# Kernel tuning notes

Hardware: AMD Instinct MI355X
Metric: run time of the kernel (lower is better)

## Reference

```python
import jax, jax.numpy as jnp
import numpy as np

N, E = 25000, 400000
D, H, L = 64, 4, 3
DH = D  # per-head out dim (concat=False averages heads)
NODE_IN, EDGE_IN = 16, 4


def setup_inputs() -> dict:
    key = jax.random.key(0)
    ks = jax.random.split(key, 24)
    s = 0.05
    inp = {
        "node_feat_in": jax.random.normal(ks[0], (N, NODE_IN), jnp.float32),
        "edge_index_in": jax.random.randint(ks[1], (2, E), 0, N, jnp.int32),
        "edge_attr_in": jax.random.normal(ks[2], (E, EDGE_IN), jnp.float32),
        # initial embeddings
        "W_node": jax.random.normal(ks[3], (NODE_IN, D), jnp.float32) * s,
        "b_node": jnp.zeros((D,), jnp.float32),
        "W_edge": jax.random.normal(ks[4], (EDGE_IN, D), jnp.float32) * s,
        "b_edge": jnp.zeros((D,), jnp.float32),
        # GATv2Conv params, stacked over layers
        "Wl": jax.random.normal(ks[5], (L, D, H * DH), jnp.float32) * s,
        "bl": jnp.zeros((L, H * DH), jnp.float32),
        "Wr": jax.random.normal(ks[6], (L, D, H * DH), jnp.float32) * s,
        "br": jnp.zeros((L, H * DH), jnp.float32),
        "We": jax.random.normal(ks[7], (L, D, H * DH), jnp.float32) * s,
        "att": jax.random.normal(ks[8], (L, H, DH), jnp.float32) * s,
        "conv_b": jnp.zeros((L, D), jnp.float32),
        # LayerNorm
        "ln_g": jnp.ones((L, D), jnp.float32),
        "ln_b": jnp.zeros((L, D), jnp.float32),
        # edge update MLP: Linear(3D->D), ReLU, Linear(D->D)
        "euW1": jax.random.normal(ks[9], (L, 3 * D, D), jnp.float32) * s,
        "eub1": jnp.zeros((L, D), jnp.float32),
        "euW2": jax.random.normal(ks[10], (L, D, D), jnp.float32) * s,
        "eub2": jnp.zeros((L, D), jnp.float32),
    }
    return inp


def _layernorm(x, g, b, eps=1e-5):
    mu = x.mean(-1, keepdims=True)
    var = ((x - mu) ** 2).mean(-1, keepdims=True)
    return (x - mu) * jax.lax.rsqrt(var + eps) * g + b


def _gatv2_conv(x, e, row, col, Wl, bl, Wr, br, We, att, cb):
    # PyG GATv2Conv(concat=False, edge_dim=D), eval mode (no dropout),
    # add_self_loops=True with fill_value='mean' on edge_attr.
    n = x.shape[0]
    xl = (x @ Wl + bl).reshape(n, H, DH)  # source transform
    xr = (x @ Wr + br).reshape(n, H, DH)  # target transform
    # self-loop edge attr = per-target mean of incoming edge attrs
    cnt = jax.ops.segment_sum(jnp.ones((e.shape[0],), x.dtype), col, num_segments=n)
    e_loop = jax.ops.segment_sum(e, col, num_segments=n) / jnp.maximum(cnt, 1.0)[:, None]
    ee = (jnp.concatenate([e, e_loop], 0) @ We).reshape(-1, H, DH)
    loop = jnp.arange(n, dtype=row.dtype)
    rowf = jnp.concatenate([row, loop])
    colf = jnp.concatenate([col, loop])
    msg = xl[rowf] + xr[colf] + ee                      # [E+N, H, DH]
    score = jnp.sum(jax.nn.leaky_relu(msg, 0.2) * att, -1)  # [E+N, H]
    # segment softmax over incoming edges of each target node
    m = jax.ops.segment_max(score, colf, num_segments=n)
    a = jnp.exp(score - m[colf])
    a = a / jax.ops.segment_sum(a, colf, num_segments=n)[colf]
    out = jax.ops.segment_sum(a[..., None] * xl[rowf], colf, num_segments=n)  # [N,H,DH]
    return out.mean(1) + cb  # concat=False -> head mean, plus bias


def reference(node_feat_in, edge_index_in, edge_attr_in, W_node, b_node, W_edge,
              b_edge, Wl, bl, Wr, br, We, att, conv_b, ln_g, ln_b, euW1, eub1,
              euW2, eub2):
    row, col = edge_index_in[0], edge_index_in[1]
    x = jax.nn.relu(node_feat_in @ W_node + b_node)
    e = jax.nn.relu(edge_attr_in @ W_edge + b_edge)
    for i in range(L):
        upd = _gatv2_conv(x, e, row, col, Wl[i], bl[i], Wr[i], br[i], We[i],
                          att[i], conv_b[i])
        x = jax.nn.relu(_layernorm(x + upd, ln_g[i], ln_b[i]))
        eu_in = jnp.concatenate([x[row], x[col], e], -1)  # [E, 3D]
        e_upd = jax.nn.relu(eu_in @ euW1[i] + eub1[i]) @ euW2[i] + eub2[i]
        e = jax.nn.relu(e + e_upd)
    return x, e
```

## Files before the change

### kernel.cpp

```cpp
#include <hip/hip_runtime.h>
#include <hip/hip_bf16.h>
#include <cstdint>
#include <cstddef>

constexpr int kN  = 25000;
constexpr int kE  = 400000;
constexpr int kEN = kE + kN;
constexpr int kD  = 64;
constexpr int kH  = 4;
constexpr int kHD = 256;

typedef __attribute__((ext_vector_type(8))) short short8;
typedef __attribute__((ext_vector_type(4))) float f32x4;

__device__ __forceinline__ float lrelu02(float x){ return x > 0.f ? x : 0.2f*x; }
__device__ __forceinline__ unsigned short f2bf(float f){
  __hip_bfloat16 h = __float2bfloat16(f);
  return *reinterpret_cast<unsigned short*>(&h);
}
__device__ __forceinline__ float bf2f(unsigned short u){
  return __uint_as_float(((unsigned)u) << 16);
}
__device__ __forceinline__ float bf_lo(unsigned u){ return __uint_as_float(u << 16); }
__device__ __forceinline__ float bf_hi(unsigned u){ return __uint_as_float(u & 0xffff0000u); }
__device__ __forceinline__ unsigned pack_bf2(float a, float b){
  return ((unsigned)f2bf(a)) | (((unsigned)f2bf(b)) << 16);
}

__global__ void k_deg(const int* __restrict__ col, int* __restrict__ deg){
  int i = blockIdx.x*256 + threadIdx.x;
  if (i < kE) atomicAdd(&deg[col[i]], 1);
}

__global__ void k_scan(const int* __restrict__ deg, int* __restrict__ col_start){
  __shared__ int lds[1024];
  __shared__ int carry_s;
  int t = threadIdx.x;
  if (t == 0) carry_s = 0;
  __syncthreads();
  for (int base = 0; base < kN; base += 1024){
    int v = (base + t < kN) ? deg[base + t] : 0;
    lds[t] = v; __syncthreads();
    for (int off = 1; off < 1024; off <<= 1){
      int add = (t >= off) ? lds[t - off] : 0;
      __syncthreads();
      lds[t] += add;
      __syncthreads();
    }
    int incl = lds[t];
    int carry = carry_s;
    if (base + t < kN) col_start[base + t] = carry + incl - v;
    __syncthreads();
    if (t == 0) carry_s = carry + lds[1023];
    __syncthreads();
  }
  if (t == 0) col_start[kN] = carry_s;
}

__global__ void k_fill(const int* __restrict__ col, const int* __restrict__ col_start,
                       int* __restrict__ fill, int* __restrict__ edge_ids){
  int i = blockIdx.x*256 + threadIdx.x;
  if (i < kE){
    int c = col[i];
    int p = atomicAdd(&fill[c], 1);
    edge_ids[col_start[c] + p] = i;
  }
}

__global__ void k_permrc(const int* __restrict__ edge_ids, const int* __restrict__ row,
                         const int* __restrict__ col, int* __restrict__ rowp,
                         int2* __restrict__ rc2){
  int p = blockIdx.x*256 + threadIdx.x;
  if (p < kE){
    int eid = edge_ids[p];
    int r = row[eid], c = col[eid];
    rowp[p] = r;
    rc2[p] = make_int2(r, c);
  }
}

__global__ void k_prep(const float* __restrict__ We, unsigned short* __restrict__ WeT){
  int idx = blockIdx.x*256 + threadIdx.x;
  if (idx >= 3*256*64) return;
  int l = idx >> 14, j = (idx >> 6) & 255, k = idx & 63;
  WeT[idx] = f2bf(We[(size_t)l*16384 + k*256 + j]);
}

__global__ void k_prep2(const float* __restrict__ euW1, const float* __restrict__ euW2,
                        unsigned short* __restrict__ W1cT, unsigned short* __restrict__ W2T){
  int idx = blockIdx.x*256 + threadIdx.x;
  if (idx >= 3*64*64) return;
  int l = idx >> 12, rem = idx & 4095, d = rem >> 6, k = rem & 63;
  W1cT[idx] = f2bf(euW1[(size_t)l*192*64 + (size_t)(128+k)*64 + d]);
  W2T[idx]  = f2bf(euW2[(size_t)l*64*64  + (size_t)k*64 + d]);
}

__global__ void k_x0(const float* __restrict__ nf, const float* __restrict__ W,
                     const float* __restrict__ b, float* __restrict__ x){
  int i = blockIdx.x*256 + threadIdx.x;
  if (i >= kN*kD) return;
  int n = i >> 6, d = i & 63;
  float acc = b[d];
#pragma unroll
  for (int k = 0; k < 16; k++) acc += nf[n*16 + k] * W[k*64 + d];
  x[i] = fmaxf(acc, 0.f);
}

__global__ void k_e0p(const int* __restrict__ edge_ids,
                      const float* __restrict__ ea, const float* __restrict__ W,
                      const float* __restrict__ b,
                      unsigned short* __restrict__ ebf_perm){
  long long i = (long long)blockIdx.x*256 + threadIdx.x;
  if (i >= (long long)kE*kD) return;
  int p = (int)(i >> 6), d = (int)(i & 63);
  int eid = edge_ids[p];
  float acc = b[d];
#pragma unroll
  for (int k = 0; k < 4; k++) acc += ea[eid*4 + k] * W[k*64 + d];
  ebf_perm[i] = f2bf(fmaxf(acc, 0.f));
}

#define XLR_NPB 8
__global__ __launch_bounds__(256) void k_xlr(const float* __restrict__ x,
    const float* __restrict__ Wl, const float* __restrict__ bl,
    const float* __restrict__ Wr, const float* __restrict__ br,
    unsigned short* __restrict__ xl_bf, unsigned short* __restrict__ xr_bf){
  __shared__ float xs[XLR_NPB*64];
  int j = threadIdx.x;
  int n0 = blockIdx.x * XLR_NPB;
  for (int i = j; i < XLR_NPB*64; i += 256){
    int n = n0 + (i >> 6);
    xs[i] = (n < kN) ? x[(size_t)n*64 + (i & 63)] : 0.f;
  }
  __syncthreads();
  float accl[XLR_NPB], accr[XLR_NPB];
  float blv = bl[j], brv = br[j];
#pragma unroll
  for (int t = 0; t < XLR_NPB; t++){ accl[t] = blv; accr[t] = brv; }
  for (int k = 0; k < 64; k++){
    float wl = Wl[k*kHD + j], wr = Wr[k*kHD + j];
#pragma unroll
    for (int t = 0; t < XLR_NPB; t++){
      float xv = xs[t*64 + k];
      accl[t] += xv * wl; accr[t] += xv * wr;
    }
  }
#pragma unroll
  for (int t = 0; t < XLR_NPB; t++){
    int n = n0 + t;
    if (n < kN){
      xl_bf[(size_t)n*kHD + j] = f2bf(accl[t]);
      xr_bf[(size_t)n*kHD + j] = f2bf(accr[t]);
    }
  }
}

__global__ __launch_bounds__(256) void k_eloop(const unsigned short* __restrict__ ebf_perm,
    const int* __restrict__ col_start, unsigned short* __restrict__ eloop_bf){
  int wave = threadIdx.x >> 6, lane = threadIdx.x & 63;
  int n = blockIdx.x*4 + wave;
  if (n >= kN) return;
  int s0 = col_start[n], s1 = col_start[n+1];
  float acc = 0.f;
  for (int p = s0; p < s1; p++)
    acc += bf2f(ebf_perm[(size_t)p*64 + lane]);
  int dg = s1 - s0;
  eloop_bf[(size_t)n*64 + lane] = f2bf(acc / (float)(dg > 0 ? dg : 1));
}

struct STile {
  short8 b0, b1;
  uint2 xlu[4], xru[4];
};

__device__ __forceinline__ void s_load(int tile, STile& f, int e16, int kb, int h,
    const unsigned short* __restrict__ ebf_perm,
    const unsigned short* __restrict__ eloop_bf,
    const unsigned short* __restrict__ xl_bf,
    const unsigned short* __restrict__ xr_bf,
    const int2* __restrict__ rc2)
{
  int p = tile*16 + e16;
  int pc = (p < kEN) ? p : 0;
  bool isE = pc < kE;
  int2 rc;
  if (isE) rc = rc2[pc];
  else { rc.x = pc - kE; rc.y = pc - kE; }
  const unsigned short* erow = isE ? (ebf_perm + (size_t)pc*64)
                                   : (eloop_bf + (size_t)(pc - kE)*64);
  f.b0 = *(const short8*)(erow + kb*8);
  f.b1 = *(const short8*)(erow + 32 + kb*8);
  const unsigned short* xl_ = xl_bf + (size_t)rc.x*kHD + h*64;
  const unsigned short* xr_ = xr_bf + (size_t)rc.y*kHD + h*64;
#pragma unroll
  for (int mt = 0; mt < 4; mt++){
    f.xlu[mt] = *(const uint2*)(xl_ + mt*16 + kb*4);
    f.xru[mt] = *(const uint2*)(xr_ + mt*16 + kb*4);
  }
}

__device__ __forceinline__ void s_comp(int tile, const STile& f,
    const short8 A[4][2], const uint2 attp[4], int lane, int h,
    float* __restrict__ score)
{
  float sc = 0.f;
#pragma unroll
  for (int mt = 0; mt < 4; mt++){
    f32x4 acc = {0.f,0.f,0.f,0.f};
    acc = __builtin_amdgcn_mfma_f32_16x16x32_bf16(A[mt][0], f.b0, acc, 0, 0, 0);
    acc = __builtin_amdgcn_mfma_f32_16x16x32_bf16(A[mt][1], f.b1, acc, 0, 0, 0);
    sc += lrelu02(acc[0] + bf_lo(f.xlu[mt].x) + bf_lo(f.xru[mt].x)) * bf_lo(attp[mt].x);
    sc += lrelu02(acc[1] + bf_hi(f.xlu[mt].x) + bf_hi(f.xru[mt].x)) * bf_hi(attp[mt].x);
    sc += lrelu02(acc[2] + bf_lo(f.xlu[mt].y) + bf_lo(f.xru[mt].y)) * bf_lo(attp[mt].y);
    sc += lrelu02(acc[3] + bf_hi(f.xlu[mt].y) + bf_hi(f.xru[mt].y)) * bf_hi(attp[mt].y);
  }
  sc += __shfl_xor(sc, 16);
  sc += __shfl_xor(sc, 32);
  int wp = tile*16 + lane;
  if (lane < 16 && wp < kEN) score[(size_t)wp*kH + h] = sc;
}

__global__ __launch_bounds__(256) void k_score_mfma(
    const unsigned short* __restrict__ ebf_perm,
    const unsigned short* __restrict__ eloop_bf,
    const unsigned short* __restrict__ xl_bf,
    const unsigned short* __restrict__ xr_bf,
    const int2* __restrict__ rc2,
    const unsigned short* __restrict__ WeT,
    const float* __restrict__ att,
    float* __restrict__ score)
{
  int lane = threadIdx.x & 63;
  int h    = threadIdx.x >> 6;
  int e16  = lane & 15;
  int kb   = lane >> 4;

  short8 A[4][2];
  uint2 attp[4];
#pragma unroll
  for (int mt = 0; mt < 4; mt++){
    const unsigned short* arow = WeT + (size_t)(h*64 + mt*16 + e16)*64 + kb*8;
    A[mt][0] = *(const short8*)(arow);
    A[mt][1] = *(const short8*)(arow + 32);
    f32x4 av = *(const f32x4*)(att + h*64 + mt*16 + kb*4);
    attp[mt].x = pack_bf2(av[0], av[1]);
    attp[mt].y = pack_bf2(av[2], av[3]);
  }

  constexpr int NT = (kEN + 15)/16;
  const int G = gridDim.x;
  STile fA, fB;
  int t0 = blockIdx.x;
  if (t0 < NT) s_load(t0, fA, e16, kb, h, ebf_perm, eloop_bf, xl_bf, xr_bf, rc2);
  for (int tile = t0; tile < NT; tile += 2*G){
    int t1 = tile + G;
    if (t1 < NT) s_load(t1, fB, e16, kb, h, ebf_perm, eloop_bf, xl_bf, xr_bf, rc2);
    s_comp(tile, fA, A, attp, lane, h, score);
    if (t1 < NT){
      int t2 = tile + 2*G;
      if (t2 < NT) s_load(t2, fA, e16, kb, h, ebf_perm, eloop_bf, xl_bf, xr_bf, rc2);
      s_comp(t1, fB, A, attp, lane, h, score);
    }
  }
}

__global__ __launch_bounds__(256) void k_agg_ln(
    const unsigned short* __restrict__ xl_bf, const float* __restrict__ score,
    const int* __restrict__ rowp, const int* __restrict__ col_start,
    const float* __restrict__ conv_b, const float* __restrict__ ln_g,
    const float* __restrict__ ln_b, float* __restrict__ x){
  int wv = threadIdx.x >> 6, l = threadIdx.x & 63;
  int n = blockIdx.x*4 + wv;
  if (n >= kN) return;
  int h = l >> 4;
  int s0 = col_start[n], s1 = col_start[n+1];

  float sc_self = score[(size_t)(kE + n)*kH + h];
  float m = sc_self;
  for (int p = s0; p < s1; p++)
    m = fmaxf(m, score[(size_t)p*kH + h]);

  float w0 = __expf(sc_self - m);
  float s = w0;
  float a0, a1, a2, a3;
  {
    uint2 u = *(const uint2*)(xl_bf + (size_t)n*kHD + l*4);
    a0 = w0*bf_lo(u.x); a1 = w0*bf_hi(u.x);
    a2 = w0*bf_lo(u.y); a3 = w0*bf_hi(u.y);
  }
  int p = s0;
  for (; p + 4 <= s1; p += 4){
    float e0 = __expf(score[(size_t)(p+0)*kH + h] - m);
    float e1 = __expf(score[(size_t)(p+1)*kH + h] - m);
    float e2 = __expf(score[(size_t)(p+2)*kH + h] - m);
    float e3 = __expf(score[(size_t)(p+3)*kH + h] - m);
    int r0 = rowp[p], r1 = rowp[p+1], r2 = rowp[p+2], r3 = rowp[p+3];
    uint2 u0 = *(const uint2*)(xl_bf + (size_t)r0*kHD + l*4);
    uint2 u1 = *(const uint2*)(xl_bf + (size_t)r1*kHD + l*4);
    uint2 u2 = *(const uint2*)(xl_bf + (size_t)r2*kHD + l*4);
    uint2 u3 = *(const uint2*)(xl_bf + (size_t)r3*kHD + l*4);
    s += e0 + e1 + e2 + e3;
    a0 += e0*bf_lo(u0.x) + e1*bf_lo(u1.x) + e2*bf_lo(u2.x) + e3*bf_lo(u3.x);
    a1 += e0*bf_hi(u0.x) + e1*bf_hi(u1.x) + e2*bf_hi(u2.x) + e3*bf_hi(u3.x);
    a2 += e0*bf_lo(u0.y) + e1*bf_lo(u1.y) + e2*bf_lo(u2.y) + e3*bf_lo(u3.y);
    a3 += e0*bf_hi(u0.y) + e1*bf_hi(u1.y) + e2*bf_hi(u2.y) + e3*bf_hi(u3.y);
  }
  for (; p < s1; p++){
    float ew = __expf(score[(size_t)p*kH + h] - m);
    int r = rowp[p];
    uint2 u = *(const uint2*)(xl_bf + (size_t)r*kHD + l*4);
    s += ew;
    a0 += ew*bf_lo(u.x); a1 += ew*bf_hi(u.x);
    a2 += ew*bf_lo(u.y); a3 += ew*bf_hi(u.y);
  }
  float inv = 1.f / s;
  a0 *= inv; a1 *= inv; a2 *= inv; a3 *= inv;
  a0 += __shfl_xor(a0, 16); a0 += __shfl_xor(a0, 32);
  a1 += __shfl_xor(a1, 16); a1 += __shfl_xor(a1, 32);
  a2 += __shfl_xor(a2, 16); a2 += __shfl_xor(a2, 32);
  a3 += __shfl_xor(a3, 16); a3 += __shfl_xor(a3, 32);
  int d0 = (l & 15)*4;
  f32x4 cb = *(const f32x4*)(conv_b + d0);
  f32x4 xv = *(const f32x4*)(x + (size_t)n*64 + d0);
  float y0 = xv[0] + a0*0.25f + cb[0];
  float y1 = xv[1] + a1*0.25f + cb[1];
  float y2 = xv[2] + a2*0.25f + cb[2];
  float y3 = xv[3] + a3*0.25f + cb[3];
  float part = y0 + y1 + y2 + y3;
  part += __shfl_xor(part, 1); part += __shfl_xor(part, 2);
  part += __shfl_xor(part, 4); part += __shfl_xor(part, 8);
  float mu = part * (1.f/64.f);
  float f0 = y0 - mu, f1 = y1 - mu, f2 = y2 - mu, f3 = y3 - mu;
  float vp = f0*f0 + f1*f1 + f2*f2 + f3*f3;
  vp += __shfl_xor(vp, 1); vp += __shfl_xor(vp, 2);
  vp += __shfl_xor(vp, 4); vp += __shfl_xor(vp, 8);
  float rstd = rsqrtf(vp * (1.f/64.f) + 1e-5f);
  f32x4 gv = *(const f32x4*)(ln_g + d0);
  f32x4 bv = *(const f32x4*)(ln_b + d0);
  if (l < 16){
    f32x4 o;
    o[0] = fmaxf(f0*rstd*gv[0] + bv[0], 0.f);
    o[1] = fmaxf(f1*rstd*gv[1] + bv[1], 0.f);
    o[2] = fmaxf(f2*rstd*gv[2] + bv[2], 0.f);
    o[3] = fmaxf(f3*rstd*gv[3] + bv[3], 0.f);
    *(f32x4*)(x + (size_t)n*64 + d0) = o;
  }
}

#define PQ_NPB 16
__global__ __launch_bounds__(256) void k_pq(const float* __restrict__ x,
    const float* __restrict__ W1, const float* __restrict__ b1,
    unsigned short* __restrict__ P_bf, unsigned short* __restrict__ Q_bf){
  __shared__ float xs[PQ_NPB*64];
  int tid = threadIdx.x;
  int j = tid & 63;
  int s = tid >> 6;
  int n0 = blockIdx.x * PQ_NPB;
  for (int i = tid; i < PQ_NPB*64; i += 256){
    int n = n0 + (i >> 6);
    xs[i] = (n < kN) ? x[(size_t)n*64 + (i & 63)] : 0.f;
  }
  __syncthreads();
  float accP[4], accQ[4];
  float b1v = b1[j];
#pragma unroll
  for (int t = 0; t < 4; t++){ accP[t] = b1v; accQ[t] = 0.f; }
  for (int k = 0; k < 64; k++){
    float wa = W1[k*64 + j];
    float wb = W1[(64 + k)*64 + j];
#pragma unroll
    for (int t = 0; t < 4; t++){
      float xv = xs[(s*4 + t)*64 + k];
      accP[t] += xv * wa; accQ[t] += xv * wb;
    }
  }
#pragma unroll
  for (int t = 0; t < 4; t++){
    int n = n0 + s*4 + t;
    if (n < kN){
      P_bf[(size_t)n*64 + j] = f2bf(accP[t]);
      Q_bf[(size_t)n*64 + j] = f2bf(accQ[t]);
    }
  }
}

__global__ __launch_bounds__(256) void k_mlp_mfma(
    unsigned short* __restrict__ ebf_perm,
    float* __restrict__ eout_scatter,
    const int* __restrict__ edge_ids,
    const unsigned short* __restrict__ P_bf, const unsigned short* __restrict__ Q_bf,
    const unsigned short* __restrict__ W1cT,
    const unsigned short* __restrict__ W2T,
    const float* __restrict__ b2,
    const int2* __restrict__ rc2)
{
  __shared__ unsigned short Hl[4][1024];
  int lane = threadIdx.x & 63, wv = threadIdx.x >> 6;
  int e16 = lane & 15, g = lane >> 4;
  int swz = (e16 & 7) << 4;
  char* Hw = (char*)Hl[wv];
  bool last = (eout_scatter != nullptr);

  short8 a1[4][2], a2[4][2];
#pragma unroll
  for (int mt = 0; mt < 4; mt++){
#pragma unroll
    for (int c = 0; c < 2; c++){
      a1[mt][c] = *(const short8*)(W1cT + (size_t)(mt*16 + e16)*64 + c*32 + g*8);
      a2[mt][c] = *(const short8*)(W2T  + (size_t)(mt*16 + e16)*64 + c*32 + g*8);
    }
  }
  f32x4 b2v[4];
#pragma unroll
  for (int mt = 0; mt < 4; mt++) b2v[mt] = *(const f32x4*)(b2 + mt*16 + g*4);

  int wid = (blockIdx.x*256 + threadIdx.x) >> 6;
  int nw  = (gridDim.x*256) >> 6;
  for (int tile = wid; tile < kE/16; tile += nw){
    int p = tile*16 + e16;
    int2 rc = rc2[p];
    const unsigned short* erow = ebf_perm + (size_t)p*64;
    short8 eb0 = *(const short8*)(erow + g*8);
    short8 eb1 = *(const short8*)(erow + 32 + g*8);
    const unsigned short* Pr = P_bf + (size_t)rc.x*64;
    const unsigned short* Qc = Q_bf + (size_t)rc.y*64;

#pragma unroll
    for (int mt = 0; mt < 4; mt++){
      f32x4 acc = {0.f,0.f,0.f,0.f};
      acc = __builtin_amdgcn_mfma_f32_16x16x32_bf16(a1[mt][0], eb0, acc, 0, 0, 0);
      acc = __builtin_amdgcn_mfma_f32_16x16x32_bf16(a1[mt][1], eb1, acc, 0, 0, 0);
      uint2 pu = *(const uint2*)(Pr + mt*16 + g*4);
      uint2 qu = *(const uint2*)(Qc + mt*16 + g*4);
      float h0 = fmaxf(acc[0] + bf_lo(pu.x) + bf_lo(qu.x), 0.f);
      float h1 = fmaxf(acc[1] + bf_hi(pu.x) + bf_hi(qu.x), 0.f);
      float h2 = fmaxf(acc[2] + bf_lo(pu.y) + bf_lo(qu.y), 0.f);
      float h3 = fmaxf(acc[3] + bf_hi(pu.y) + bf_hi(qu.y), 0.f);
      uint2 pk; pk.x = pack_bf2(h0, h1); pk.y = pack_bf2(h2, h3);
      *(uint2*)(Hw + (((e16 << 7) + (mt << 5) + (g << 3)) ^ swz)) = pk;
    }
    short8 hb0 = *(const short8*)(Hw + (((e16 << 7)      + (g << 4)) ^ swz));
    short8 hb1 = *(const short8*)(Hw + (((e16 << 7) + 64 + (g << 4)) ^ swz));

    int oe = last ? edge_ids[p] : 0;
#pragma unroll
    for (int mt = 0; mt < 4; mt++){
      f32x4 o = {0.f,0.f,0.f,0.f};
      o = __builtin_amdgcn_mfma_f32_16x16x32_bf16(a2[mt][0], hb0, o, 0, 0, 0);
      o = __builtin_amdgcn_mfma_f32_16x16x32_bf16(a2[mt][1], hb1, o, 0, 0, 0);
      size_t off = (size_t)p*64 + mt*16 + g*4;
      uint2 u = *(const uint2*)(ebf_perm + off);
      f32x4 eo;
      eo[0] = bf_lo(u.x); eo[1] = bf_hi(u.x); eo[2] = bf_lo(u.y); eo[3] = bf_hi(u.y);
      f32x4 ne;
      ne[0] = fmaxf(eo[0] + o[0] + b2v[mt][0], 0.f);
      ne[1] = fmaxf(eo[1] + o[1] + b2v[mt][1], 0.f);
      ne[2] = fmaxf(eo[2] + o[2] + b2v[mt][2], 0.f);
      ne[3] = fmaxf(eo[3] + o[3] + b2v[mt][3], 0.f);
      if (!last){
        uint2 po; po.x = pack_bf2(ne[0], ne[1]); po.y = pack_bf2(ne[2], ne[3]);
        *(uint2*)(ebf_perm + off) = po;
      } else {
        *(f32x4*)(eout_scatter + (size_t)oe*64 + mt*16 + g*4) = ne;
      }
    }
  }
}

extern "C" void kernel_launch(void* const* d_in, const int* in_sizes, int n_in,
                              void* d_out, int out_size, void* d_ws, size_t ws_size,
                              hipStream_t stream) {
  const float* node_feat = (const float*)d_in[0];
  const int*   edge_idx  = (const int*)d_in[1];
  const float* edge_attr = (const float*)d_in[2];
  const float* W_node = (const float*)d_in[3];
  const float* b_node = (const float*)d_in[4];
  const float* W_edge = (const float*)d_in[5];
  const float* b_edge = (const float*)d_in[6];
  const float* Wl   = (const float*)d_in[7];
  const float* bl   = (const float*)d_in[8];
  const float* Wr   = (const float*)d_in[9];
  const float* br   = (const float*)d_in[10];
  const float* We   = (const float*)d_in[11];
  const float* att  = (const float*)d_in[12];
  const float* cvb  = (const float*)d_in[13];
  const float* lng  = (const float*)d_in[14];
  const float* lnb  = (const float*)d_in[15];
  const float* euW1 = (const float*)d_in[16];
  const float* eub1 = (const float*)d_in[17];
  const float* euW2 = (const float*)d_in[18];
  const float* eub2 = (const float*)d_in[19];

  const int* row = edge_idx;
  const int* col = edge_idx + kE;

  float* x = (float*)d_out;
  float* e_out = (float*)d_out + (size_t)kN*kD;

  char* p = (char*)d_ws;
  auto carve = [&](size_t bytes)->void*{
    void* r = (void*)p;
    p += (bytes + 255) & ~(size_t)255;
    return r;
  };
  unsigned short* xl_bf    = (unsigned short*)carve((size_t)kN*kHD*2);
  unsigned short* xr_bf    = (unsigned short*)carve((size_t)kN*kHD*2);
  unsigned short* P_bf     = (unsigned short*)carve((size_t)kN*kD*2);
  unsigned short* Q_bf     = (unsigned short*)carve((size_t)kN*kD*2);
  unsigned short* ebf_perm = (unsigned short*)carve((size_t)kE*kD*2);
  unsigned short* eloop_bf = (unsigned short*)carve((size_t)kN*kD*2);
  unsigned short* WeT      = (unsigned short*)carve((size_t)3*kHD*kD*2);
  unsigned short* W1cT     = (unsigned short*)carve((size_t)3*kD*kD*2);
  unsigned short* W2T      = (unsigned short*)carve((size_t)3*kD*kD*2);
  float* score  = (float*)carve((size_t)kEN*kH*4);
  int* deg      = (int*)carve((size_t)kN*4);
  int* col_start= (int*)carve((size_t)(kN+1)*4);
  int* fill     = (int*)carve((size_t)kN*4);
  int* edge_ids = (int*)carve((size_t)kE*4);
  int* rowp     = (int*)carve((size_t)kE*4);
  int2* rc2     = (int2*)carve((size_t)kE*8);

  hipMemsetAsync(deg, 0, (size_t)kN*4, stream);
  hipMemsetAsync(fill, 0, (size_t)kN*4, stream);
  k_deg<<<(kE+255)/256, 256, 0, stream>>>(col, deg);
  k_scan<<<1, 1024, 0, stream>>>(deg, col_start);
  k_fill<<<(kE+255)/256, 256, 0, stream>>>(col, col_start, fill, edge_ids);
  k_permrc<<<(kE+255)/256, 256, 0, stream>>>(edge_ids, row, col, rowp, rc2);

  k_prep<<<192, 256, 0, stream>>>(We, WeT);
  k_prep2<<<48, 256, 0, stream>>>(euW1, euW2, W1cT, W2T);
  k_x0<<<(kN*kD+255)/256, 256, 0, stream>>>(node_feat, W_node, b_node, x);
  k_e0p<<<(int)(((size_t)kE*kD+255)/256), 256, 0, stream>>>(edge_ids, edge_attr, W_edge,
                                                            b_edge, ebf_perm);

  for (int i = 0; i < 3; i++){
    const float* Wl_i  = Wl  + (size_t)i*kD*kHD;
    const float* bl_i  = bl  + (size_t)i*kHD;
    const float* Wr_i  = Wr  + (size_t)i*kD*kHD;
    const float* br_i  = br  + (size_t)i*kHD;
    const float* att_i = att + (size_t)i*kHD;
    const float* cvb_i = cvb + (size_t)i*kD;
    const float* lng_i = lng + (size_t)i*kD;
    const float* lnb_i = lnb + (size_t)i*kD;
    const float* W1_i  = euW1 + (size_t)i*192*64;
    const float* b1_i  = eub1 + (size_t)i*kD;
    const float* b2_i  = eub2 + (size_t)i*kD;
    const unsigned short* WeT_i  = WeT  + (size_t)i*kHD*kD;
    const unsigned short* W1cT_i = W1cT + (size_t)i*kD*kD;
    const unsigned short* W2T_i  = W2T  + (size_t)i*kD*kD;

    k_xlr<<<(kN + XLR_NPB - 1)/XLR_NPB, 256, 0, stream>>>(x, Wl_i, bl_i, Wr_i, br_i,
                                                          xl_bf, xr_bf);
    k_eloop<<<(kN + 3)/4, 256, 0, stream>>>(ebf_perm, col_start, eloop_bf);
    k_score_mfma<<<2048, 256, 0, stream>>>(ebf_perm, eloop_bf, xl_bf, xr_bf,
                                           rc2, WeT_i, att_i, score);
    k_agg_ln<<<(kN + 3)/4, 256, 0, stream>>>(xl_bf, score, rowp, col_start,
                                             cvb_i, lng_i, lnb_i, x);
    k_pq<<<(kN + PQ_NPB - 1)/PQ_NPB, 256, 0, stream>>>(x, W1_i, b1_i, P_bf, Q_bf);
    k_mlp_mfma<<<2048, 256, 0, stream>>>(ebf_perm, (i < 2) ? nullptr : e_out,
                                         edge_ids, P_bf, Q_bf, W1cT_i, W2T_i, b2_i,
                                         rc2);
  }
}
```

Measured before the change: 986.1 us.

## Fuse next-layer xl/xr projection with P/Q and remap score waves per XCD

Merges the P/Q projection kernel with the next layer's xl/xr projection so x is loaded once per node block and one launch per layer is removed; the first layer's xl/xr is computed before the loop. The score kernel now assigns each head to a pair of XCDs based on block id and has each wave stride independently over tiles, dropping the software double-buffered loads. This trades load prefetch overlap and cross-head sharing of tile data for a simpler loop and head-local weights per XCD.

```diff
diff --git a/kernel.cpp b/kernel.cpp
--- a/kernel.cpp
+++ b/kernel.cpp
@@ -151,6 +151,68 @@
     if (n < kN){
       xl_bf[(size_t)n*kHD + j] = f2bf(accl[t]);
       xr_bf[(size_t)n*kHD + j] = f2bf(accr[t]);
+    }
+  }
+}
+
+__global__ __launch_bounds__(256) void k_xlrpq(const float* __restrict__ x,
+    const float* __restrict__ Wl, const float* __restrict__ bl,
+    const float* __restrict__ Wr, const float* __restrict__ br,
+    const float* __restrict__ W1, const float* __restrict__ b1,
+    int do_xlr,
+    unsigned short* __restrict__ xl_bf, unsigned short* __restrict__ xr_bf,
+    unsigned short* __restrict__ P_bf, unsigned short* __restrict__ Q_bf){
+  __shared__ float xs[XLR_NPB*64];
+  int j = threadIdx.x;
+  int n0 = blockIdx.x * XLR_NPB;
+  for (int i = j; i < XLR_NPB*64; i += 256){
+    int n = n0 + (i >> 6);
+    xs[i] = (n < kN) ? x[(size_t)n*64 + (i & 63)] : 0.f;
+  }
+  __syncthreads();
+
+  int jc = j & 63, s = j >> 6;
+  int tb = (s & 1)*4;
+  bool isQ = (s >= 2);
+  float accpq[4];
+  float b1v = isQ ? 0.f : b1[jc];
+#pragma unroll
+  for (int t = 0; t < 4; t++) accpq[t] = b1v;
+  const float* Wpq = W1 + (isQ ? 64*64 : 0);
+  for (int k = 0; k < 64; k++){
+    float w = Wpq[k*64 + jc];
+#pragma unroll
+    for (int t = 0; t < 4; t++) accpq[t] += xs[(tb + t)*64 + k] * w;
+  }
+#pragma unroll
+  for (int t = 0; t < 4; t++){
+    int n = n0 + tb + t;
+    if (n < kN){
+      if (isQ) Q_bf[(size_t)n*64 + jc] = f2bf(accpq[t]);
+      else     P_bf[(size_t)n*64 + jc] = f2bf(accpq[t]);
+    }
+  }
+
+  if (do_xlr){
+    float accl[XLR_NPB], accr[XLR_NPB];
+    float blv = bl[j], brv = br[j];
+#pragma unroll
+    for (int t = 0; t < XLR_NPB; t++){ accl[t] = blv; accr[t] = brv; }
+    for (int k = 0; k < 64; k++){
+      float wl = Wl[k*kHD + j], wr = Wr[k*kHD + j];
+#pragma unroll
+      for (int t = 0; t < XLR_NPB; t++){
+        float xv = xs[t*64 + k];
+        accl[t] += xv * wl; accr[t] += xv * wr;
+      }
+    }
+#pragma unroll
+    for (int t = 0; t < XLR_NPB; t++){
+      int n = n0 + t;
+      if (n < kN){
+        xl_bf[(size_t)n*kHD + j] = f2bf(accl[t]);
+        xr_bf[(size_t)n*kHD + j] = f2bf(accr[t]);
+      }
     }
   }
 }
@@ -231,9 +293,15 @@
     float* __restrict__ score)
 {
   int lane = threadIdx.x & 63;
-  int h    = threadIdx.x >> 6;
+  int wv   = threadIdx.x >> 6;
   int e16  = lane & 15;
   int kb   = lane >> 4;
+
+  int b = blockIdx.x;
+  int xcd = b & 7;
+  int h = xcd >> 1;
+  int sub = ((b >> 3) << 1) | (xcd & 1);
+  int wid = sub*4 + wv;
 
   short8 A[4][2];
   uint2 attp[4];
@@ -248,19 +316,10 @@
   }
 
   constexpr int NT = (kEN + 15)/16;
-  const int G = gridDim.x;
-  STile fA, fB;
-  int t0 = blockIdx.x;
-  if (t0 < NT) s_load(t0, fA, e16, kb, h, ebf_perm, eloop_bf, xl_bf, xr_bf, rc2);
-  for (int tile = t0; tile < NT; tile += 2*G){
-    int t1 = tile + G;
-    if (t1 < NT) s_load(t1, fB, e16, kb, h, ebf_perm, eloop_bf, xl_bf, xr_bf, rc2);
-    s_comp(tile, fA, A, attp, lane, h, score);
-    if (t1 < NT){
-      int t2 = tile + 2*G;
-      if (t2 < NT) s_load(t2, fA, e16, kb, h, ebf_perm, eloop_bf, xl_bf, xr_bf, rc2);
-      s_comp(t1, fB, A, attp, lane, h, score);
-    }
+  for (int tile = wid; tile < NT; tile += 2048){
+    STile f;
+    s_load(tile, f, e16, kb, h, ebf_perm, eloop_bf, xl_bf, xr_bf, rc2);
+    s_comp(tile, f, A, attp, lane, h, score);
   }
 }
 
@@ -347,43 +406,6 @@
   }
 }
 
-#define PQ_NPB 16
-__global__ __launch_bounds__(256) void k_pq(const float* __restrict__ x,
-    const float* __restrict__ W1, const float* __restrict__ b1,
-    unsigned short* __restrict__ P_bf, unsigned short* __restrict__ Q_bf){
-  __shared__ float xs[PQ_NPB*64];
-  int tid = threadIdx.x;
-  int j = tid & 63;
-  int s = tid >> 6;
-  int n0 = blockIdx.x * PQ_NPB;
-  for (int i = tid; i < PQ_NPB*64; i += 256){
-    int n = n0 + (i >> 6);
-    xs[i] = (n < kN) ? x[(size_t)n*64 + (i & 63)] : 0.f;
-  }
-  __syncthreads();
-  float accP[4], accQ[4];
-  float b1v = b1[j];
-#pragma unroll
-  for (int t = 0; t < 4; t++){ accP[t] = b1v; accQ[t] = 0.f; }
-  for (int k = 0; k < 64; k++){
-    float wa = W1[k*64 + j];
-    float wb = W1[(64 + k)*64 + j];
-#pragma unroll
-    for (int t = 0; t < 4; t++){
-      float xv = xs[(s*4 + t)*64 + k];
-      accP[t] += xv * wa; accQ[t] += xv * wb;
-    }
-  }
-#pragma unroll
-  for (int t = 0; t < 4; t++){
-    int n = n0 + s*4 + t;
-    if (n < kN){
-      P_bf[(size_t)n*64 + j] = f2bf(accP[t]);
-      Q_bf[(size_t)n*64 + j] = f2bf(accQ[t]);
-    }
-  }
-}
-
 __global__ __launch_bounds__(256) void k_mlp_mfma(
     unsigned short* __restrict__ ebf_perm,
     float* __restrict__ eout_scatter,
@@ -532,12 +554,9 @@
   k_x0<<<(kN*kD+255)/256, 256, 0, stream>>>(node_feat, W_node, b_node, x);
   k_e0p<<<(int)(((size_t)kE*kD+255)/256), 256, 0, stream>>>(edge_ids, edge_attr, W_edge,
                                                             b_edge, ebf_perm);
+  k_xlr<<<(kN + XLR_NPB - 1)/XLR_NPB, 256, 0, stream>>>(x, Wl, bl, Wr, br, xl_bf, xr_bf);
 
   for (int i = 0; i < 3; i++){
-    const float* Wl_i  = Wl  + (size_t)i*kD*kHD;
-    const float* bl_i  = bl  + (size_t)i*kHD;
-    const float* Wr_i  = Wr  + (size_t)i*kD*kHD;
-    const float* br_i  = br  + (size_t)i*kHD;
     const float* att_i = att + (size_t)i*kHD;
     const float* cvb_i = cvb + (size_t)i*kD;
     const float* lng_i = lng + (size_t)i*kD;
@@ -548,15 +567,20 @@
     const unsigned short* WeT_i  = WeT  + (size_t)i*kHD*kD;
     const unsigned short* W1cT_i = W1cT + (size_t)i*kD*kD;
     const unsigned short* W2T_i  = W2T  + (size_t)i*kD*kD;
-
-    k_xlr<<<(kN + XLR_NPB - 1)/XLR_NPB, 256, 0, stream>>>(x, Wl_i, bl_i, Wr_i, br_i,
-                                                          xl_bf, xr_bf);
+    int ni = (i < 2) ? (i + 1) : 0;
+    const float* Wl_n = Wl + (size_t)ni*kD*kHD;
+    const float* bl_n = bl + (size_t)ni*kHD;
+    const float* Wr_n = Wr + (size_t)ni*kD*kHD;
+    const float* br_n = br + (size_t)ni*kHD;
+
     k_eloop<<<(kN + 3)/4, 256, 0, stream>>>(ebf_perm, col_start, eloop_bf);
     k_score_mfma<<<2048, 256, 0, stream>>>(ebf_perm, eloop_bf, xl_bf, xr_bf,
                                            rc2, WeT_i, att_i, score);
     k_agg_ln<<<(kN + 3)/4, 256, 0, stream>>>(xl_bf, score, rowp, col_start,
                                              cvb_i, lng_i, lnb_i, x);
-    k_pq<<<(kN + PQ_NPB - 1)/PQ_NPB, 256, 0, stream>>>(x, W1_i, b1_i, P_bf, Q_bf);
+    k_xlrpq<<<(kN + XLR_NPB - 1)/XLR_NPB, 256, 0, stream>>>(x, Wl_n, bl_n, Wr_n, br_n,
+                                                            W1_i, b1_i, (i < 2) ? 1 : 0,
+                                                            xl_bf, xr_bf, P_bf, Q_bf);
     k_mlp_mfma<<<2048, 256, 0, stream>>>(ebf_perm, (i < 2) ? nullptr : e_out,
                                          edge_ids, P_bf, Q_bf, W1cT_i, W2T_i, b2_i,
                                          rc2);
```

Result: slower. 1.079 ms (+9.5%).
